# Optimization experiments

Hardware: AMD Instinct MI355X
Metric: run time of the kernel (lower is better)

The kernel has to match this reference:

```python
import jax, jax.numpy as jnp
import numpy as np

N_NODES = 512
N_VEC = 8          # n_vectors_hidden
N_FEAT = 128       # n_invariant_feat_hidden
MLP_UNITS = [128, 128]


def _mlp(x, Ws):
    # e3nn-style MLP on scalars: no bias, weights scaled by 1/sqrt(fan_in), silu on every layer
    for W in Ws:
        x = jax.nn.silu(x @ W / jnp.sqrt(jnp.asarray(W.shape[0], x.dtype)))
    return x


def setup_inputs() -> dict:
    key = jax.random.key(0)
    ks = jax.random.split(key, 12)
    d_edge = N_VEC + 2 * N_FEAT  # 264
    inp = {
        "positions": jax.random.normal(ks[0], (N_NODES, N_VEC, 3), jnp.float32),
        "features": jax.random.normal(ks[1], (N_NODES, N_FEAT), jnp.float32),
        # phi_e
        "We1": jax.random.normal(ks[2], (d_edge, MLP_UNITS[0]), jnp.float32),
        "We2": jax.random.normal(ks[3], (MLP_UNITS[0], MLP_UNITS[1]), jnp.float32),
        # phi_x
        "Wx1": jax.random.normal(ks[4], (MLP_UNITS[1], MLP_UNITS[0]), jnp.float32),
        "Wx2": jax.random.normal(ks[5], (MLP_UNITS[0], MLP_UNITS[1]), jnp.float32),
        # phi_inf
        "Winf": jax.random.normal(ks[6], (MLP_UNITS[1], 1), jnp.float32),
        # FullyConnectedTensorProduct weights: [scalar_mul, sh_mul, out_mul]
        "Wtp": jax.random.normal(ks[7], (MLP_UNITS[1], N_VEC, N_VEC), jnp.float32),
        # phi_h + final linear
        "Wh1": jax.random.normal(ks[8], (MLP_UNITS[1] + N_FEAT, MLP_UNITS[0]), jnp.float32),
        "Wh2": jax.random.normal(ks[9], (MLP_UNITS[0], MLP_UNITS[1]), jnp.float32),
        "Wh3": jax.random.normal(ks[10], (MLP_UNITS[1], N_FEAT), jnp.float32),
    }
    return inp


def reference(positions, features, We1, We2, Wx1, Wx2, Winf, Wtp, Wh1, Wh2, Wh3):
    n, V, _ = positions.shape
    # fully-connected edge list (senders sorted, self-loops excluded)
    idx = np.arange(n)
    senders = np.repeat(idx, n - 1)                                  # [E]
    receivers = (senders + np.tile(np.arange(1, n), n)) % n          # [E]

    vectors = positions[senders] - positions[receivers]              # [E,V,3]
    sq = jnp.sum(vectors * vectors, axis=-1)
    lengths = jnp.sqrt(jnp.maximum(sq, 1e-20))                       # safe_norm [E,V]

    edge_feat = jnp.concatenate(
        [lengths, features[senders], features[receivers]], axis=-1)  # [E, V+2F]
    m_ij = _mlp(edge_feat, [We1, We2])                               # [E, U]
    phi_x_out = _mlp(m_ij, [Wx1, Wx2])                               # [E, U]

    unit = vectors / lengths[..., None]                              # [E,V,3]
    sh1 = jnp.sqrt(jnp.asarray(3.0, unit.dtype)) * unit              # ell=1, component norm
    # FCTP: only 0e (x) 1o -> 1o path reaches the n_vectors x 1o output
    U = phi_x_out.shape[-1]
    norm = jnp.sqrt(jnp.asarray(U * V, sh1.dtype))
    out_vec = jnp.einsum('uvw,eu,evk->ewk', Wtp, phi_x_out, sh1) / norm  # [E,W,3]

    vector_per_node = jax.ops.segment_sum(out_vec, senders, num_segments=n)  # [n,W,3]

    e = jax.nn.sigmoid(m_ij @ Winf / jnp.sqrt(jnp.asarray(Winf.shape[0], m_ij.dtype)))  # [E,1]
    m_i = jax.ops.segment_sum(m_ij * e, senders, num_segments=n)     # [n,U]

    h = _mlp(jnp.concatenate([m_i, features], axis=-1), [Wh1, Wh2])
    h = h @ Wh3 / jnp.sqrt(jnp.asarray(Wh3.shape[0], h.dtype))       # final linear -> F
    features_out = h + features                                      # residual_h
    positions_out = positions + vector_per_node
    return positions_out, features_out
```

## Files before the change

kernel.cpp:

```cpp
#include <hip/hip_runtime.h>
#include <math.h>

#define NN   512
#define NV   8
#define CH   32
#define NCHH 8

#define C1 0.06154574548966636f
#define C2 0.08838834764831845f
#define SQRT3 1.7320508075688772f

typedef __attribute__((ext_vector_type(8))) short bf16x8;
typedef __attribute__((ext_vector_type(4))) float f32x4;

#define MFMA16 __builtin_amdgcn_mfma_f32_16x16x32_bf16
#define CVT_PK(dst, a, b) asm("v_cvt_pk_bf16_f32 %0, %1, %2" : "=v"(dst) : "v"(a), "v"(b))

__device__ __forceinline__ float silu_f(float x) {
    float e = __builtin_amdgcn_exp2f(x * -1.442695041f);
    return x * __builtin_amdgcn_rcpf(1.0f + e);
}
__device__ __forceinline__ float sigm_f(float x) {
    float e = __builtin_amdgcn_exp2f(x * -1.442695041f);
    return __builtin_amdgcn_rcpf(1.0f + e);
}
__device__ __forceinline__ short f2bf(float f) {
    unsigned u = __builtin_bit_cast(unsigned, f);
    u = (u + 0x7FFFu + ((u >> 16) & 1u)) >> 16;
    return (short)u;
}
__device__ __forceinline__ float bfhi(unsigned u) {
    return __builtin_bit_cast(float, u & 0xFFFF0000u);
}
__device__ __forceinline__ float bflo(unsigned u) {
    return __builtin_bit_cast(float, u << 16);
}

__device__ __forceinline__ void packW(const float* __restrict__ W,
                                      short* __restrict__ out, int ncols, int ct)
{
    int t = threadIdx.x;
    int lane = t & 63, kt = (t >> 6) & 3;
    int g = lane >> 4, c = lane & 15;
    bf16x8 v;
    #pragma unroll
    for (int j = 0; j < 8; ++j)
        v[j] = f2bf(W[(kt * 32 + g * 8 + j) * ncols + ct * 16 + c]);
    *(bf16x8*)(out + (size_t)(ct * 256 + t) * 8) = v;
}

__global__ __launch_bounds__(256)
void k_packall(const float* __restrict__ We2, const float* __restrict__ Wx1,
               const float* __restrict__ Wx2, const float* __restrict__ Wtp,
               const float* __restrict__ We1, const float* __restrict__ feat,
               short* __restrict__ We2p, short* __restrict__ Wx1p,
               short* __restrict__ Wx2p, short* __restrict__ Wtpp,
               short* __restrict__ We1Lp,
               float* __restrict__ FsP, float* __restrict__ FrP)
{
    const int b = blockIdx.x, t = threadIdx.x;
    if (b < 8)       { packW(We2, We2p, 128, b);      return; }
    if (b < 16)      { packW(Wx1, Wx1p, 128, b - 8);  return; }
    if (b < 24)      { packW(Wx2, Wx2p, 128, b - 16); return; }
    if (b < 28)      { packW(Wtp, Wtpp,  64, b - 24); return; }
    if (b == 28) {
        #pragma unroll
        for (int h = 0; h < 2; ++h) {
            int tt = t + h * 256;
            int ct = tt >> 6, l = tt & 63, g = l >> 4, c = l & 15;
            bf16x8 v = {0,0,0,0,0,0,0,0};
            if (g == 0) {
                #pragma unroll
                for (int j = 0; j < 8; ++j)
                    v[j] = f2bf(We1[j * 128 + ct * 16 + c]);
            }
            *(bf16x8*)(We1Lp + (size_t)tt * 8) = v;
        }
        return;
    }
    __shared__ float sF[256];
    const int n = (b - 29) * 2 + (t >> 7), j = t & 127, hb = t & 128;
    sF[t] = feat[n * 128 + j];
    __syncthreads();
    float a = 0.f, bb = 0.f;
    #pragma unroll 8
    for (int k = 0; k < 128; ++k) {
        float f = sF[hb + k];
        a  = fmaf(f, We1[(8   + k) * 128 + j], a);
        bb = fmaf(f, We1[(136 + k) * 128 + j], bb);
    }
    FsP[n * 128 + j] = a;
    FrP[n * 128 + j] = bb;
}

__device__ __forceinline__ void loadBz(const short* __restrict__ p,
                                       bf16x8 (&B)[2][4], int w, int lane)
{
    int zz = 0; asm volatile("" : "+v"(zz));
    const bf16x8* p8 = (const bf16x8*)p;
    #pragma unroll
    for (int ctl = 0; ctl < 2; ++ctl)
        #pragma unroll
        for (int kt = 0; kt < 4; ++kt)
            B[ctl][kt] = p8[((w * 2 + ctl) * 4 + kt) * 64 + lane + zz];
}

__device__ __forceinline__ void gemm_mfma(const short* sIn_, const bf16x8 (&B)[2][4],
                                          const int (&adrK)[4], f32x4 (&acc)[2][2])
{
    const char* sIn = (const char*)sIn_;
    const f32x4 z = {0.f, 0.f, 0.f, 0.f};
    acc[0][0] = z; acc[0][1] = z; acc[1][0] = z; acc[1][1] = z;
    #pragma unroll
    for (int kt = 0; kt < 4; ++kt) {
        bf16x8 a0 = *(const bf16x8*)(sIn + adrK[kt]);
        bf16x8 a1 = *(const bf16x8*)(sIn + adrK[kt] + 4096);
        acc[0][0] = MFMA16(a0, B[0][kt], acc[0][0], 0, 0, 0);
        acc[0][1] = MFMA16(a0, B[1][kt], acc[0][1], 0, 0, 0);
        acc[1][0] = MFMA16(a1, B[0][kt], acc[1][0], 0, 0, 0);
        acc[1][1] = MFMA16(a1, B[1][kt], acc[1][1], 0, 0, 0);
    }
}

template<bool KEEP>
__device__ __forceinline__ void epi_store(const f32x4 (&acc)[2][2], short* sOut_,
                                          const int (&wAdr)[2][4], float scale,
                                          f32x4 (&keep)[2][2])
{
    char* sOut = (char*)sOut_;
    #pragma unroll
    for (int rt = 0; rt < 2; ++rt)
        #pragma unroll
        for (int ctl = 0; ctl < 2; ++ctl) {
            float v0 = silu_f(acc[rt][ctl][0] * scale);
            float v1 = silu_f(acc[rt][ctl][1] * scale);
            float v2 = silu_f(acc[rt][ctl][2] * scale);
            float v3 = silu_f(acc[rt][ctl][3] * scale);
            if (KEEP) {
                keep[rt][ctl][0] = v0; keep[rt][ctl][1] = v1;
                keep[rt][ctl][2] = v2; keep[rt][ctl][3] = v3;
            }
            unsigned p01, p23;
            CVT_PK(p01, v0, v1);
            CVT_PK(p23, v2, v3);
            char* o = sOut + rt * 4096;
            *(short*)(o + wAdr[ctl][0]) = (short)(p01 & 0xFFFFu);
            *(short*)(o + wAdr[ctl][1]) = (short)(p01 >> 16);
            *(short*)(o + wAdr[ctl][2]) = (short)(p23 & 0xFFFFu);
            *(short*)(o + wAdr[ctl][3]) = (short)(p23 >> 16);
        }
}

__global__ __launch_bounds__(256, 4)
void k_edge(const float* __restrict__ pos,
            const float* __restrict__ Winf,
            const float* __restrict__ FsP,
            const float* __restrict__ FrP,
            const short* __restrict__ We1Lp,
            const short* __restrict__ We2p,
            const short* __restrict__ Wx1p,
            const short* __restrict__ Wx2p,
            const short* __restrict__ Wtpp,
            float* __restrict__ MI2,
            float* __restrict__ VEC2)
{
    __shared__ __align__(16) short sX[CH * 128];
    __shared__ __align__(16) short sY[CH * 128];
    __shared__ __align__(16) float sLS[CH * NV * 4];
    __shared__ float sWinf[8 * 17];
    __shared__ float sPosS[24];
    __shared__ float sE[CH];
    __shared__ float sVp[4 * 24];

    const int bid = blockIdx.x;
    const int s = bid >> 1, half = bid & 1;
    const int t = threadIdx.x;
    const int lane = t & 63, w = t >> 6;
    const int rl = lane & 15, kg = lane >> 4;

    const int swz = (rl & 7) << 4;
    const int ktperm = (rl & 4) << 4;
    const int baseRd = rl * 256 + ((kg * 16) ^ (swz & 0x30));
    int adrK[4];
    #pragma unroll
    for (int kt = 0; kt < 4; ++kt) adrK[kt] = baseRd + ((kt * 64) ^ ktperm);
    int wAdr[2][4];
    #pragma unroll
    for (int ctl = 0; ctl < 2; ++ctl)
        #pragma unroll
        for (int jj = 0; jj < 4; ++jj) {
            int r = kg * 4 + jj;
            wAdr[ctl][jj] = r * 256 + ((w * 64 + ctl * 32 + 2 * rl) ^ ((r & 7) << 4));
        }
    const int colg0 = w * 32 + rl, colg1 = colg0 + 16;
    const int er = t >> 3, eo = t & 7;
    const int eAdr0 = er * 256 + ((eo * 32)      ^ ((er & 7) << 4));
    const int eAdr1 = er * 256 + ((eo * 32 + 16) ^ ((er & 7) << 4));
    const int vv = w * 2 + (rl >> 3);

    if (t < 128) sWinf[(t >> 4) * 17 + (t & 15)] = Winf[t];
    if (t < 24)  sPosS[t] = pos[s * 24 + t];

    const float fs0 = FsP[s * 128 + colg0];
    const float fs1 = FsP[s * 128 + colg1];

    float miacc0 = 0.f, miacc1 = 0.f;
    float vax = 0.f, vay = 0.f, vaz = 0.f;
    __syncthreads();

    for (int c = 0; c < NCHH; ++c) {
        const int r0 = (half * NCHH + c) * CH;

        bf16x8 Bw[2][4];
        loadBz(We2p, Bw, w, lane);
        bf16x8 bL0, bL1;
        {
            int zz = 0; asm volatile("" : "+v"(zz));
            const bf16x8* pL = (const bf16x8*)We1Lp;
            bL0 = pL[(w * 2 + 0) * 64 + lane + zz];
            bL1 = pL[(w * 2 + 1) * 64 + lane + zz];
        }
        float frv[2][2][4];
        {
            int zz = 0; asm volatile("" : "+v"(zz));
            #pragma unroll
            for (int rt = 0; rt < 2; ++rt)
                #pragma unroll
                for (int jj = 0; jj < 4; ++jj) {
                    const float* fp = FrP + (size_t)(r0 + rt * 16 + kg * 4 + jj) * 128 + zz;
                    frv[rt][0][jj] = fp[colg0];
                    frv[rt][1][jj] = fp[colg1];
                }
        }

        {
            int r = t >> 3, v = t & 7;
            const float* pr = pos + (size_t)(r0 + r) * 24 + v * 3;
            float dx = sPosS[v * 3 + 0] - pr[0];
            float dy = sPosS[v * 3 + 1] - pr[1];
            float dz = sPosS[v * 3 + 2] - pr[2];
            float sq  = dx * dx + dy * dy + dz * dz;
            float len = sqrtf(fmaxf(sq, 1e-20f));
            float inv = SQRT3 / len;
            f32x4 o; o[0] = dx * inv; o[1] = dy * inv; o[2] = dz * inv; o[3] = len;
            *(f32x4*)(sLS + (r * 8 + (v ^ (r & 7))) * 4) = o;
        }
        __syncthreads();

        {
            bf16x8 aL0 = {0,0,0,0,0,0,0,0}, aL1 = {0,0,0,0,0,0,0,0};
            if (kg == 0) {
                const float* Lp = sLS + rl * 32;
                const float* Lq = sLS + (rl + 16) * 32;
                unsigned u0[4], u1[4];
                #pragma unroll
                for (int jp = 0; jp < 4; ++jp) {
                    CVT_PK(u0[jp], Lp[((2*jp)   ^ (rl & 7)) * 4 + 3],
                                   Lp[((2*jp+1) ^ (rl & 7)) * 4 + 3]);
                    CVT_PK(u1[jp], Lq[((2*jp)   ^ (rl & 7)) * 4 + 3],
                                   Lq[((2*jp+1) ^ (rl & 7)) * 4 + 3]);
                }
                uint4 v0 = {u0[0], u0[1], u0[2], u0[3]};
                uint4 v1 = {u1[0], u1[1], u1[2], u1[3]};
                aL0 = __builtin_bit_cast(bf16x8, v0);
                aL1 = __builtin_bit_cast(bf16x8, v1);
            }
            const f32x4 z = {0.f, 0.f, 0.f, 0.f};
            f32x4 aP[2][2];
            aP[0][0] = MFMA16(aL0, bL0, z, 0, 0, 0);
            aP[0][1] = MFMA16(aL0, bL1, z, 0, 0, 0);
            aP[1][0] = MFMA16(aL1, bL0, z, 0, 0, 0);
            aP[1][1] = MFMA16(aL1, bL1, z, 0, 0, 0);
            char* sXc = (char*)sX;
            #pragma unroll
            for (int rt = 0; rt < 2; ++rt)
                #pragma unroll
                for (int ctl = 0; ctl < 2; ++ctl) {
                    float fsv = ctl ? fs1 : fs0;
                    float v0 = silu_f((aP[rt][ctl][0] + fsv + frv[rt][ctl][0]) * C1);
                    float v1 = silu_f((aP[rt][ctl][1] + fsv + frv[rt][ctl][1]) * C1);
                    float v2 = silu_f((aP[rt][ctl][2] + fsv + frv[rt][ctl][2]) * C1);
                    float v3 = silu_f((aP[rt][ctl][3] + fsv + frv[rt][ctl][3]) * C1);
                    unsigned p01, p23;
                    CVT_PK(p01, v0, v1);
                    CVT_PK(p23, v2, v3);
                    char* o = sXc + rt * 4096;
                    *(short*)(o + wAdr[ctl][0]) = (short)(p01 & 0xFFFFu);
                    *(short*)(o + wAdr[ctl][1]) = (short)(p01 >> 16);
                    *(short*)(o + wAdr[ctl][2]) = (short)(p23 & 0xFFFFu);
                    *(short*)(o + wAdr[ctl][3]) = (short)(p23 >> 16);
                }
        }
        __syncthreads();

        f32x4 acc[2][2];
        f32x4 keepM[2][2];
        gemm_mfma(sX, Bw, adrK, acc);
        bf16x8 Bn[2][4];
        loadBz(Wx1p, Bn, w, lane);
        epi_store<true>(acc, sY, wAdr, C2, keepM);
        __syncthreads();

        {
            const char* sYc = (const char*)sY;
            uint4 m0 = *(const uint4*)(sYc + eAdr0);
            uint4 m1 = *(const uint4*)(sYc + eAdr1);
            const unsigned mu[8] = {m0.x, m0.y, m0.z, m0.w, m1.x, m1.y, m1.z, m1.w};
            float d = 0.f;
            #pragma unroll
            for (int q = 0; q < 8; ++q) {
                d = fmaf(bflo(mu[q]), sWinf[eo * 17 + 2 * q],     d);
                d = fmaf(bfhi(mu[q]), sWinf[eo * 17 + 2 * q + 1], d);
            }
            d += __shfl_xor(d, 1); d += __shfl_xor(d, 2); d += __shfl_xor(d, 4);
            if (eo == 0) sE[er] = (r0 + er == s) ? 0.f : sigm_f(d * C2);
        }
        __syncthreads();

        #pragma unroll
        for (int rt = 0; rt < 2; ++rt)
            #pragma unroll
            for (int jj = 0; jj < 4; ++jj) {
                float e = sE[rt * 16 + kg * 4 + jj];
                miacc0 = fmaf(keepM[rt][0][jj], e, miacc0);
                miacc1 = fmaf(keepM[rt][1][jj], e, miacc1);
            }

        gemm_mfma(sY, Bn, adrK, acc);
        loadBz(Wx2p, Bw, w, lane);
        epi_store<false>(acc, sX, wAdr, C2, keepM);
        __syncthreads();

        gemm_mfma(sX, Bw, adrK, acc);
        bf16x8 Bt[4];
        {
            int zz = 0; asm volatile("" : "+v"(zz));
            const bf16x8* p8 = (const bf16x8*)Wtpp;
            #pragma unroll
            for (int kt = 0; kt < 4; ++kt) Bt[kt] = p8[(w * 4 + kt) * 64 + lane + zz];
        }
        epi_store<false>(acc, sY, wAdr, C2, keepM);
        __syncthreads();

        {
            const f32x4 z = {0.f, 0.f, 0.f, 0.f};
            f32x4 acc0 = z, acc1 = z;
            const char* sYc = (const char*)sY;
            #pragma unroll
            for (int kt = 0; kt < 4; ++kt) {
                bf16x8 a0 = *(const bf16x8*)(sYc + adrK[kt]);
                bf16x8 a1 = *(const bf16x8*)(sYc + adrK[kt] + 4096);
                acc0 = MFMA16(a0, Bt[kt], acc0, 0, 0, 0);
                acc1 = MFMA16(a1, Bt[kt], acc1, 0, 0, 0);
            }
            #pragma unroll
            for (int rt = 0; rt < 2; ++rt)
                #pragma unroll
                for (int jj = 0; jj < 4; ++jj) {
                    int row = rt * 16 + kg * 4 + jj;
                    const f32x4 sh = *(const f32x4*)(sLS + (row * 8 + (vv ^ (row & 7))) * 4);
                    float g = rt ? acc1[jj] : acc0[jj];
                    vax = fmaf(g, sh[0], vax);
                    vay = fmaf(g, sh[1], vay);
                    vaz = fmaf(g, sh[2], vaz);
                }
        }
        __syncthreads();
    }

    miacc0 += __shfl_xor(miacc0, 16); miacc0 += __shfl_xor(miacc0, 32);
    miacc1 += __shfl_xor(miacc1, 16); miacc1 += __shfl_xor(miacc1, 32);
    if (lane < 16) {
        float* mo = MI2 + (size_t)(half * NN + s) * 128;
        mo[w * 32 + lane]      = miacc0;
        mo[w * 32 + 16 + lane] = miacc1;
    }
    vax += __shfl_xor(vax, 8);  vay += __shfl_xor(vay, 8);  vaz += __shfl_xor(vaz, 8);
    vax += __shfl_xor(vax, 16); vay += __shfl_xor(vay, 16); vaz += __shfl_xor(vaz, 16);
    vax += __shfl_xor(vax, 32); vay += __shfl_xor(vay, 32); vaz += __shfl_xor(vaz, 32);
    if ((lane & 56) == 0) {
        float* vp = sVp + w * 24 + lane * 3;
        vp[0] = vax; vp[1] = vay; vp[2] = vaz;
    }
    __syncthreads();
    if (t < 24) {
        float sum = sVp[t] + sVp[24 + t] + sVp[48 + t] + sVp[72 + t];
        VEC2[(size_t)(half * NN + s) * 24 + t] = sum * (1.0f / 32.0f);
    }
}

__global__ __launch_bounds__(128)
void k_node(const float* __restrict__ pos, const float* __restrict__ feat,
            const float* __restrict__ Wh1, const float* __restrict__ Wh2,
            const float* __restrict__ Wh3,
            const float* __restrict__ MI2, const float* __restrict__ VEC2,
            float* __restrict__ outPos, float* __restrict__ outFeat)
{
    __shared__ float sMi[128], sF[128], sH[128];
    int n = blockIdx.x, j = threadIdx.x;
    sMi[j] = MI2[n * 128 + j] + MI2[NN * 128 + n * 128 + j];
    sF[j]  = feat[n * 128 + j];
    __syncthreads();
    float a = 0.f;
    #pragma unroll 8
    for (int k = 0; k < 128; ++k) a = fmaf(sMi[k], Wh1[k * 128 + j], a);
    #pragma unroll 8
    for (int k = 0; k < 128; ++k) a = fmaf(sF[k], Wh1[(128 + k) * 128 + j], a);
    a = silu_f(a * 0.0625f);
    sH[j] = a;
    __syncthreads();
    float b = 0.f;
    #pragma unroll 8
    for (int k = 0; k < 128; ++k) b = fmaf(sH[k], Wh2[k * 128 + j], b);
    b = silu_f(b * C2);
    sMi[j] = b;
    __syncthreads();
    float cc = 0.f;
    #pragma unroll 8
    for (int k = 0; k < 128; ++k) cc = fmaf(sMi[k], Wh3[k * 128 + j], cc);
    outFeat[n * 128 + j] = cc * C2 + sF[j];
    if (j < 24) outPos[n * 24 + j] = pos[n * 24 + j]
                                   + VEC2[n * 24 + j] + VEC2[NN * 24 + n * 24 + j];
}

extern "C" void kernel_launch(void* const* d_in, const int* in_sizes, int n_in,
                              void* d_out, int out_size, void* d_ws, size_t ws_size,
                              hipStream_t stream) {
    const float* pos  = (const float*)d_in[0];
    const float* feat = (const float*)d_in[1];
    const float* We1  = (const float*)d_in[2];
    const float* We2  = (const float*)d_in[3];
    const float* Wx1  = (const float*)d_in[4];
    const float* Wx2  = (const float*)d_in[5];
    const float* Winf = (const float*)d_in[6];
    const float* Wtp  = (const float*)d_in[7];
    const float* Wh1  = (const float*)d_in[8];
    const float* Wh2  = (const float*)d_in[9];
    const float* Wh3  = (const float*)d_in[10];

    float* outPos  = (float*)d_out;
    float* outFeat = (float*)d_out + NN * 24;

    float* ws   = (float*)d_ws;
    float* FsP  = ws;
    float* FrP  = ws + 65536;
    float* MI2  = ws + 131072;
    float* VEC2 = ws + 262144;
    short* wpack = (short*)(ws + 286720);
    short* We2p  = wpack;
    short* Wx1p  = wpack + 16384;
    short* Wx2p  = wpack + 32768;
    short* Wtpp  = wpack + 49152;
    short* We1Lp = wpack + 57344;

    k_packall<<<dim3(285), dim3(256), 0, stream>>>(We2, Wx1, Wx2, Wtp, We1, feat,
                                                   We2p, Wx1p, Wx2p, Wtpp, We1Lp,
                                                   FsP, FrP);
    k_edge<<<dim3(2 * NN), dim3(256), 0, stream>>>(pos, Winf, FsP, FrP, We1Lp,
                                                   We2p, Wx1p, Wx2p, Wtpp, MI2, VEC2);
    k_node<<<dim3(NN), dim3(128), 0, stream>>>(pos, feat, Wh1, Wh2, Wh3, MI2, VEC2,
                                               outPos, outFeat);
}
```

Measured before the change: 96.16 us.

## Fold MLP scales into packed weights, fuse Winf gate into MFMA, drop barriers

The 1/sqrt(fan_in) scales, and the TP normalisation, are now folded into the bf16-packed weights and FsP/FrP, so the per-element multiplies in the epilogues go away. The edge gate (m_ij·Winf) is computed with extra MFMAs alongside the Wx1 GEMM instead of a separate LDS dot product, which removes two __syncthreads and the sE buffer. Each wave now computes its own copy of the lengths and unit vectors with vectorised loads and rsq, so the sLS barrier and the end-of-chunk barrier can be dropped. MFMA sections are wrapped in s_setprio. The cost is redundant geometry work per wave, 4x the LDS for sLS, and slightly different bf16 rounding because scales are applied before conversion.

```diff
diff --git a/kernel.cpp b/kernel.cpp
--- a/kernel.cpp
+++ b/kernel.cpp
@@ -2,7 +2,6 @@
 #include <math.h>
 
 #define NN   512
-#define NV   8
 #define CH   32
 #define NCHH 8
 
@@ -29,15 +28,10 @@
     u = (u + 0x7FFFu + ((u >> 16) & 1u)) >> 16;
     return (short)u;
 }
-__device__ __forceinline__ float bfhi(unsigned u) {
-    return __builtin_bit_cast(float, u & 0xFFFF0000u);
-}
-__device__ __forceinline__ float bflo(unsigned u) {
-    return __builtin_bit_cast(float, u << 16);
-}
 
 __device__ __forceinline__ void packW(const float* __restrict__ W,
-                                      short* __restrict__ out, int ncols, int ct)
+                                      short* __restrict__ out, int ncols, int ct,
+                                      float scale)
 {
     int t = threadIdx.x;
     int lane = t & 63, kt = (t >> 6) & 3;
@@ -45,24 +39,25 @@
     bf16x8 v;
     #pragma unroll
     for (int j = 0; j < 8; ++j)
-        v[j] = f2bf(W[(kt * 32 + g * 8 + j) * ncols + ct * 16 + c]);
+        v[j] = f2bf(W[(kt * 32 + g * 8 + j) * ncols + ct * 16 + c] * scale);
     *(bf16x8*)(out + (size_t)(ct * 256 + t) * 8) = v;
 }
 
 __global__ __launch_bounds__(256)
 void k_packall(const float* __restrict__ We2, const float* __restrict__ Wx1,
                const float* __restrict__ Wx2, const float* __restrict__ Wtp,
-               const float* __restrict__ We1, const float* __restrict__ feat,
+               const float* __restrict__ We1, const float* __restrict__ Winf,
+               const float* __restrict__ feat,
                short* __restrict__ We2p, short* __restrict__ Wx1p,
                short* __restrict__ Wx2p, short* __restrict__ Wtpp,
-               short* __restrict__ We1Lp,
+               short* __restrict__ We1Lp, short* __restrict__ BWinfp,
                float* __restrict__ FsP, float* __restrict__ FrP)
 {
     const int b = blockIdx.x, t = threadIdx.x;
-    if (b < 8)       { packW(We2, We2p, 128, b);      return; }
-    if (b < 16)      { packW(Wx1, Wx1p, 128, b - 8);  return; }
-    if (b < 24)      { packW(Wx2, Wx2p, 128, b - 16); return; }
-    if (b < 28)      { packW(Wtp, Wtpp,  64, b - 24); return; }
+    if (b < 8)  { packW(We2, We2p, 128, b,      C2);       return; }
+    if (b < 16) { packW(Wx1, Wx1p, 128, b - 8,  C2);       return; }
+    if (b < 24) { packW(Wx2, Wx2p, 128, b - 16, C2);       return; }
+    if (b < 28) { packW(Wtp, Wtpp,  64, b - 24, 0.03125f); return; }
     if (b == 28) {
         #pragma unroll
         for (int h = 0; h < 2; ++h) {
@@ -72,9 +67,17 @@
             if (g == 0) {
                 #pragma unroll
                 for (int j = 0; j < 8; ++j)
-                    v[j] = f2bf(We1[j * 128 + ct * 16 + c]);
+                    v[j] = f2bf(We1[j * 128 + ct * 16 + c] * C1);
             }
             *(bf16x8*)(We1Lp + (size_t)tt * 8) = v;
+        }
+        {
+            int kt = t >> 6, l = t & 63, g = l >> 4;
+            bf16x8 v;
+            #pragma unroll
+            for (int j = 0; j < 8; ++j)
+                v[j] = f2bf(Winf[kt * 32 + g * 8 + j] * C2);
+            *(bf16x8*)(BWinfp + (size_t)t * 8) = v;
         }
         return;
     }
@@ -89,8 +92,8 @@
         a  = fmaf(f, We1[(8   + k) * 128 + j], a);
         bb = fmaf(f, We1[(136 + k) * 128 + j], bb);
     }
-    FsP[n * 128 + j] = a;
-    FrP[n * 128 + j] = bb;
+    FsP[n * 128 + j] = a * C1;
+    FrP[n * 128 + j] = bb * C1;
 }
 
 __device__ __forceinline__ void loadBz(const short* __restrict__ p,
@@ -111,6 +114,7 @@
     const char* sIn = (const char*)sIn_;
     const f32x4 z = {0.f, 0.f, 0.f, 0.f};
     acc[0][0] = z; acc[0][1] = z; acc[1][0] = z; acc[1][1] = z;
+    __builtin_amdgcn_s_setprio(1);
     #pragma unroll
     for (int kt = 0; kt < 4; ++kt) {
         bf16x8 a0 = *(const bf16x8*)(sIn + adrK[kt]);
@@ -120,22 +124,22 @@
         acc[1][0] = MFMA16(a1, B[0][kt], acc[1][0], 0, 0, 0);
         acc[1][1] = MFMA16(a1, B[1][kt], acc[1][1], 0, 0, 0);
     }
+    __builtin_amdgcn_s_setprio(0);
 }
 
 template<bool KEEP>
 __device__ __forceinline__ void epi_store(const f32x4 (&acc)[2][2], short* sOut_,
-                                          const int (&wAdr)[2][4], float scale,
-                                          f32x4 (&keep)[2][2])
+                                          const int (&wAdr)[2][4], f32x4 (&keep)[2][2])
 {
     char* sOut = (char*)sOut_;
     #pragma unroll
     for (int rt = 0; rt < 2; ++rt)
         #pragma unroll
         for (int ctl = 0; ctl < 2; ++ctl) {
-            float v0 = silu_f(acc[rt][ctl][0] * scale);
-            float v1 = silu_f(acc[rt][ctl][1] * scale);
-            float v2 = silu_f(acc[rt][ctl][2] * scale);
-            float v3 = silu_f(acc[rt][ctl][3] * scale);
+            float v0 = silu_f(acc[rt][ctl][0]);
+            float v1 = silu_f(acc[rt][ctl][1]);
+            float v2 = silu_f(acc[rt][ctl][2]);
+            float v3 = silu_f(acc[rt][ctl][3]);
             if (KEEP) {
                 keep[rt][ctl][0] = v0; keep[rt][ctl][1] = v1;
                 keep[rt][ctl][2] = v2; keep[rt][ctl][3] = v3;
@@ -153,7 +157,6 @@
 
 __global__ __launch_bounds__(256, 4)
 void k_edge(const float* __restrict__ pos,
-            const float* __restrict__ Winf,
             const float* __restrict__ FsP,
             const float* __restrict__ FrP,
             const short* __restrict__ We1Lp,
@@ -161,15 +164,14 @@
             const short* __restrict__ Wx1p,
             const short* __restrict__ Wx2p,
             const short* __restrict__ Wtpp,
+            const short* __restrict__ BWinfp,
             float* __restrict__ MI2,
             float* __restrict__ VEC2)
 {
     __shared__ __align__(16) short sX[CH * 128];
     __shared__ __align__(16) short sY[CH * 128];
-    __shared__ __align__(16) float sLS[CH * NV * 4];
-    __shared__ float sWinf[8 * 17];
+    __shared__ __align__(16) float sLS[4 * 1024];
     __shared__ float sPosS[24];
-    __shared__ float sE[CH];
     __shared__ float sVp[4 * 24];
 
     const int bid = blockIdx.x;
@@ -193,19 +195,24 @@
             wAdr[ctl][jj] = r * 256 + ((w * 64 + ctl * 32 + 2 * rl) ^ ((r & 7) << 4));
         }
     const int colg0 = w * 32 + rl, colg1 = colg0 + 16;
-    const int er = t >> 3, eo = t & 7;
-    const int eAdr0 = er * 256 + ((eo * 32)      ^ ((er & 7) << 4));
-    const int eAdr1 = er * 256 + ((eo * 32 + 16) ^ ((er & 7) << 4));
     const int vv = w * 2 + (rl >> 3);
-
-    if (t < 128) sWinf[(t >> 4) * 17 + (t & 15)] = Winf[t];
-    if (t < 24)  sPosS[t] = pos[s * 24 + t];
+    float* myLS = sLS + w * 1024;
+
+    if (t < 24) sPosS[t] = pos[s * 24 + t];
 
     const float fs0 = FsP[s * 128 + colg0];
     const float fs1 = FsP[s * 128 + colg1];
 
+    bf16x8 BW[4];
+    {
+        const bf16x8* p8 = (const bf16x8*)BWinfp;
+        #pragma unroll
+        for (int kt = 0; kt < 4; ++kt) BW[kt] = p8[kt * 64 + lane];
+    }
+
     float miacc0 = 0.f, miacc1 = 0.f;
     float vax = 0.f, vay = 0.f, vaz = 0.f;
+    const f32x4 z4 = {0.f, 0.f, 0.f, 0.f};
     __syncthreads();
 
     for (int c = 0; c < NCHH; ++c) {
@@ -220,7 +227,7 @@
             bL0 = pL[(w * 2 + 0) * 64 + lane + zz];
             bL1 = pL[(w * 2 + 1) * 64 + lane + zz];
         }
-        float frv[2][2][4];
+        f32x4 cIn[2][2];
         {
             int zz = 0; asm volatile("" : "+v"(zz));
             #pragma unroll
@@ -228,30 +235,47 @@
                 #pragma unroll
                 for (int jj = 0; jj < 4; ++jj) {
                     const float* fp = FrP + (size_t)(r0 + rt * 16 + kg * 4 + jj) * 128 + zz;
-                    frv[rt][0][jj] = fp[colg0];
-                    frv[rt][1][jj] = fp[colg1];
+                    cIn[rt][0][jj] = fp[colg0] + fs0;
+                    cIn[rt][1][jj] = fp[colg1] + fs1;
                 }
         }
 
         {
-            int r = t >> 3, v = t & 7;
-            const float* pr = pos + (size_t)(r0 + r) * 24 + v * 3;
-            float dx = sPosS[v * 3 + 0] - pr[0];
-            float dy = sPosS[v * 3 + 1] - pr[1];
-            float dz = sPosS[v * 3 + 2] - pr[2];
-            float sq  = dx * dx + dy * dy + dz * dz;
-            float len = sqrtf(fmaxf(sq, 1e-20f));
-            float inv = SQRT3 / len;
-            f32x4 o; o[0] = dx * inv; o[1] = dy * inv; o[2] = dz * inv; o[3] = len;
-            *(f32x4*)(sLS + (r * 8 + (v ^ (r & 7))) * 4) = o;
-        }
-        __syncthreads();
+            int r = lane & 31, vb = lane >> 5;
+            const float* pp = pos + (size_t)(r0 + r) * 24 + vb * 12;
+            float4 q0 = *(const float4*)pp;
+            float4 q1 = *(const float4*)(pp + 4);
+            float4 q2 = *(const float4*)(pp + 8);
+            const float* sp = sPosS + vb * 12;
+            float4 s0 = *(const float4*)sp;
+            float4 s1 = *(const float4*)(sp + 4);
+            float4 s2 = *(const float4*)(sp + 8);
+            float prx[4] = {q0.x, q0.w, q1.z, q2.y};
+            float pry[4] = {q0.y, q1.x, q1.w, q2.z};
+            float prz[4] = {q0.z, q1.y, q2.x, q2.w};
+            float ssx[4] = {s0.x, s0.w, s1.z, s2.y};
+            float ssy[4] = {s0.y, s1.x, s1.w, s2.z};
+            float ssz[4] = {s0.z, s1.y, s2.x, s2.w};
+            #pragma unroll
+            for (int i = 0; i < 4; ++i) {
+                float dx = ssx[i] - prx[i];
+                float dy = ssy[i] - pry[i];
+                float dz = ssz[i] - prz[i];
+                float sq = fmaxf(dx*dx + dy*dy + dz*dz, 1e-20f);
+                float rs = __builtin_amdgcn_rsqf(sq);
+                float len = sq * rs;
+                float inv = SQRT3 * rs;
+                f32x4 o; o[0] = dx*inv; o[1] = dy*inv; o[2] = dz*inv; o[3] = len;
+                int v = vb * 4 + i;
+                *(f32x4*)(myLS + (r * 8 + (v ^ (r & 7))) * 4) = o;
+            }
+        }
 
         {
             bf16x8 aL0 = {0,0,0,0,0,0,0,0}, aL1 = {0,0,0,0,0,0,0,0};
             if (kg == 0) {
-                const float* Lp = sLS + rl * 32;
-                const float* Lq = sLS + (rl + 16) * 32;
+                const float* Lp = myLS + rl * 32;
+                const float* Lq = myLS + (rl + 16) * 32;
                 unsigned u0[4], u1[4];
                 #pragma unroll
                 for (int jp = 0; jp < 4; ++jp) {
@@ -265,70 +289,55 @@
                 aL0 = __builtin_bit_cast(bf16x8, v0);
                 aL1 = __builtin_bit_cast(bf16x8, v1);
             }
-            const f32x4 z = {0.f, 0.f, 0.f, 0.f};
             f32x4 aP[2][2];
-            aP[0][0] = MFMA16(aL0, bL0, z, 0, 0, 0);
-            aP[0][1] = MFMA16(aL0, bL1, z, 0, 0, 0);
-            aP[1][0] = MFMA16(aL1, bL0, z, 0, 0, 0);
-            aP[1][1] = MFMA16(aL1, bL1, z, 0, 0, 0);
-            char* sXc = (char*)sX;
-            #pragma unroll
-            for (int rt = 0; rt < 2; ++rt)
-                #pragma unroll
-                for (int ctl = 0; ctl < 2; ++ctl) {
-                    float fsv = ctl ? fs1 : fs0;
-                    float v0 = silu_f((aP[rt][ctl][0] + fsv + frv[rt][ctl][0]) * C1);
-                    float v1 = silu_f((aP[rt][ctl][1] + fsv + frv[rt][ctl][1]) * C1);
-                    float v2 = silu_f((aP[rt][ctl][2] + fsv + frv[rt][ctl][2]) * C1);
-                    float v3 = silu_f((aP[rt][ctl][3] + fsv + frv[rt][ctl][3]) * C1);
-                    unsigned p01, p23;
-                    CVT_PK(p01, v0, v1);
-                    CVT_PK(p23, v2, v3);
-                    char* o = sXc + rt * 4096;
-                    *(short*)(o + wAdr[ctl][0]) = (short)(p01 & 0xFFFFu);
-                    *(short*)(o + wAdr[ctl][1]) = (short)(p01 >> 16);
-                    *(short*)(o + wAdr[ctl][2]) = (short)(p23 & 0xFFFFu);
-                    *(short*)(o + wAdr[ctl][3]) = (short)(p23 >> 16);
-                }
+            aP[0][0] = MFMA16(aL0, bL0, cIn[0][0], 0, 0, 0);
+            aP[0][1] = MFMA16(aL0, bL1, cIn[0][1], 0, 0, 0);
+            aP[1][0] = MFMA16(aL1, bL0, cIn[1][0], 0, 0, 0);
+            aP[1][1] = MFMA16(aL1, bL1, cIn[1][1], 0, 0, 0);
+            f32x4 dummy[2][2];
+            epi_store<false>(aP, sX, wAdr, dummy);
         }
         __syncthreads();
 
-        f32x4 acc[2][2];
-        f32x4 keepM[2][2];
+        f32x4 acc[2][2], keepM[2][2];
         gemm_mfma(sX, Bw, adrK, acc);
         bf16x8 Bn[2][4];
         loadBz(Wx1p, Bn, w, lane);
-        epi_store<true>(acc, sY, wAdr, C2, keepM);
+        epi_store<true>(acc, sY, wAdr, keepM);
         __syncthreads();
 
+        f32x4 eacc0 = z4, eacc1 = z4;
         {
             const char* sYc = (const char*)sY;
-            uint4 m0 = *(const uint4*)(sYc + eAdr0);
-            uint4 m1 = *(const uint4*)(sYc + eAdr1);
-            const unsigned mu[8] = {m0.x, m0.y, m0.z, m0.w, m1.x, m1.y, m1.z, m1.w};
-            float d = 0.f;
-            #pragma unroll
-            for (int q = 0; q < 8; ++q) {
-                d = fmaf(bflo(mu[q]), sWinf[eo * 17 + 2 * q],     d);
-                d = fmaf(bfhi(mu[q]), sWinf[eo * 17 + 2 * q + 1], d);
-            }
-            d += __shfl_xor(d, 1); d += __shfl_xor(d, 2); d += __shfl_xor(d, 4);
-            if (eo == 0) sE[er] = (r0 + er == s) ? 0.f : sigm_f(d * C2);
-        }
-        __syncthreads();
-
-        #pragma unroll
-        for (int rt = 0; rt < 2; ++rt)
+            const f32x4 z = z4;
+            acc[0][0] = z; acc[0][1] = z; acc[1][0] = z; acc[1][1] = z;
+            __builtin_amdgcn_s_setprio(1);
+            #pragma unroll
+            for (int kt = 0; kt < 4; ++kt) {
+                bf16x8 a0 = *(const bf16x8*)(sYc + adrK[kt]);
+                bf16x8 a1 = *(const bf16x8*)(sYc + adrK[kt] + 4096);
+                acc[0][0] = MFMA16(a0, Bn[0][kt], acc[0][0], 0, 0, 0);
+                acc[0][1] = MFMA16(a0, Bn[1][kt], acc[0][1], 0, 0, 0);
+                acc[1][0] = MFMA16(a1, Bn[0][kt], acc[1][0], 0, 0, 0);
+                acc[1][1] = MFMA16(a1, Bn[1][kt], acc[1][1], 0, 0, 0);
+                eacc0 = MFMA16(a0, BW[kt], eacc0, 0, 0, 0);
+                eacc1 = MFMA16(a1, BW[kt], eacc1, 0, 0, 0);
+            }
+            __builtin_amdgcn_s_setprio(0);
+        }
+        {
+            const int sl = s - r0;
             #pragma unroll
             for (int jj = 0; jj < 4; ++jj) {
-                float e = sE[rt * 16 + kg * 4 + jj];
-                miacc0 = fmaf(keepM[rt][0][jj], e, miacc0);
-                miacc1 = fmaf(keepM[rt][1][jj], e, miacc1);
-            }
-
-        gemm_mfma(sY, Bn, adrK, acc);
+                int row = kg * 4 + jj;
+                float e0 = (row == sl)      ? 0.f : sigm_f(eacc0[jj]);
+                float e1 = (row + 16 == sl) ? 0.f : sigm_f(eacc1[jj]);
+                miacc0 = fmaf(keepM[0][0][jj], e0, fmaf(keepM[1][0][jj], e1, miacc0));
+                miacc1 = fmaf(keepM[0][1][jj], e0, fmaf(keepM[1][1][jj], e1, miacc1));
+            }
+        }
         loadBz(Wx2p, Bw, w, lane);
-        epi_store<false>(acc, sX, wAdr, C2, keepM);
+        epi_store<false>(acc, sX, wAdr, keepM);
         __syncthreads();
 
         gemm_mfma(sX, Bw, adrK, acc);
@@ -339,13 +348,13 @@
             #pragma unroll
             for (int kt = 0; kt < 4; ++kt) Bt[kt] = p8[(w * 4 + kt) * 64 + lane + zz];
         }
-        epi_store<false>(acc, sY, wAdr, C2, keepM);
+        epi_store<false>(acc, sY, wAdr, keepM);
         __syncthreads();
 
         {
-            const f32x4 z = {0.f, 0.f, 0.f, 0.f};
-            f32x4 acc0 = z, acc1 = z;
+            f32x4 acc0 = z4, acc1 = z4;
             const char* sYc = (const char*)sY;
+            __builtin_amdgcn_s_setprio(1);
             #pragma unroll
             for (int kt = 0; kt < 4; ++kt) {
                 bf16x8 a0 = *(const bf16x8*)(sYc + adrK[kt]);
@@ -353,19 +362,19 @@
                 acc0 = MFMA16(a0, Bt[kt], acc0, 0, 0, 0);
                 acc1 = MFMA16(a1, Bt[kt], acc1, 0, 0, 0);
             }
+            __builtin_amdgcn_s_setprio(0);
             #pragma unroll
             for (int rt = 0; rt < 2; ++rt)
                 #pragma unroll
                 for (int jj = 0; jj < 4; ++jj) {
                     int row = rt * 16 + kg * 4 + jj;
-                    const f32x4 sh = *(const f32x4*)(sLS + (row * 8 + (vv ^ (row & 7))) * 4);
+                    const f32x4 sh = *(const f32x4*)(myLS + (row * 8 + (vv ^ (row & 7))) * 4);
                     float g = rt ? acc1[jj] : acc0[jj];
                     vax = fmaf(g, sh[0], vax);
                     vay = fmaf(g, sh[1], vay);
                     vaz = fmaf(g, sh[2], vaz);
                 }
         }
-        __syncthreads();
     }
 
     miacc0 += __shfl_xor(miacc0, 16); miacc0 += __shfl_xor(miacc0, 32);
@@ -385,7 +394,7 @@
     __syncthreads();
     if (t < 24) {
         float sum = sVp[t] + sVp[24 + t] + sVp[48 + t] + sVp[72 + t];
-        VEC2[(size_t)(half * NN + s) * 24 + t] = sum * (1.0f / 32.0f);
+        VEC2[(size_t)(half * NN + s) * 24 + t] = sum;
     }
 }
 
@@ -446,18 +455,20 @@
     float* FrP  = ws + 65536;
     float* MI2  = ws + 131072;
     float* VEC2 = ws + 262144;
-    short* wpack = (short*)(ws + 286720);
-    short* We2p  = wpack;
-    short* Wx1p  = wpack + 16384;
-    short* Wx2p  = wpack + 32768;
-    short* Wtpp  = wpack + 49152;
-    short* We1Lp = wpack + 57344;
-
-    k_packall<<<dim3(285), dim3(256), 0, stream>>>(We2, Wx1, Wx2, Wtp, We1, feat,
+    short* wpack  = (short*)(ws + 286720);
+    short* We2p   = wpack;
+    short* Wx1p   = wpack + 16384;
+    short* Wx2p   = wpack + 32768;
+    short* Wtpp   = wpack + 49152;
+    short* We1Lp  = wpack + 57344;
+    short* BWinfp = wpack + 61440;
+
+    k_packall<<<dim3(285), dim3(256), 0, stream>>>(We2, Wx1, Wx2, Wtp, We1, Winf, feat,
                                                    We2p, Wx1p, Wx2p, Wtpp, We1Lp,
-                                                   FsP, FrP);
-    k_edge<<<dim3(2 * NN), dim3(256), 0, stream>>>(pos, Winf, FsP, FrP, We1Lp,
-                                                   We2p, Wx1p, Wx2p, Wtpp, MI2, VEC2);
+                                                   BWinfp, FsP, FrP);
+    k_edge<<<dim3(2 * NN), dim3(256), 0, stream>>>(pos, FsP, FrP, We1Lp,
+                                                   We2p, Wx1p, Wx2p, Wtpp, BWinfp,
+                                                   MI2, VEC2);
     k_node<<<dim3(NN), dim3(128), 0, stream>>>(pos, feat, Wh1, Wh2, Wh3, MI2, VEC2,
                                                outPos, outFeat);
 }
```

Result: slower. 131.8 us (+37.0%).
